# Performance work log

Measured on AMD Instinct MI355X. Metric: run time of the kernel, lower is better.

## Reference

```python
import jax, jax.numpy as jnp
import numpy as np

N_NODES = 100000


def gcn_conv(x, edge_index, edge_weight, W, b):
    """PyG GCNConv: out = D^-1/2 (A + I) D^-1/2 X W + b (self-loop weight 1)."""
    n = x.shape[0]
    src, dst = edge_index[0], edge_index[1]
    loop = jnp.arange(n)
    src_sl = jnp.concatenate([src, loop])
    dst_sl = jnp.concatenate([dst, loop])
    ew_sl = jnp.concatenate([edge_weight, jnp.ones((n,), x.dtype)])
    deg = jax.ops.segment_sum(ew_sl, dst_sl, num_segments=n)  # [N]
    dinv = jnp.where(deg > 0, jax.lax.rsqrt(deg), 0.0)
    norm = dinv[src_sl] * ew_sl * dinv[dst_sl]  # [E+N]
    h = x @ W  # [N, out_dim] dense transform before propagation
    msg = h[src_sl] * norm[:, None]  # gather + scale, [E+N, out_dim]
    out = jax.ops.segment_sum(msg, dst_sl, num_segments=n)  # scatter-add
    return out + b


def setup_inputs() -> dict:
    key = jax.random.key(0)
    ks = jax.random.split(key, 9)
    in_dim, hidden, latent = 128, 64, 32
    n, e = N_NODES, 1600000
    x = jax.random.normal(ks[0], (n, in_dim), dtype=jnp.float32)
    edge_index = jax.random.randint(ks[1], (2, e), 0, n, dtype=jnp.int64)
    edge_weight = jax.random.uniform(ks[2], (e,), dtype=jnp.float32)
    def glorot(k, fan_in, fan_out):
        s = jnp.sqrt(6.0 / (fan_in + fan_out))
        return jax.random.uniform(k, (fan_in, fan_out), jnp.float32, -s, s)
    return {
        "x": x,
        "edge_index": edge_index,
        "edge_weight": edge_weight,
        "W1": glorot(ks[3], in_dim, hidden),
        "b1": jnp.zeros((hidden,), jnp.float32),
        "W_mu": glorot(ks[4], hidden, latent),
        "b_mu": jnp.zeros((latent,), jnp.float32),
        "W_lv": glorot(ks[5], hidden, latent),
        "b_lv": jnp.zeros((latent,), jnp.float32),
    }


def reference(x, edge_index, edge_weight, W1, b1, W_mu, b_mu, W_lv, b_lv):
    h = jax.nn.relu(gcn_conv(x, edge_index, edge_weight, W1, b1))
    mu = gcn_conv(h, edge_index, edge_weight, W_mu, b_mu)
    logvar = gcn_conv(h, edge_index, edge_weight, W_lv, b_lv)
    return (mu, logvar)
```

## Files before the change

### kernel.cpp

```cpp
#include <hip/hip_runtime.h>

static __device__ __forceinline__ float4 ld4(const float* p) { return *(const float4*)p; }
static __device__ __forceinline__ float b2f(unsigned short u) {
    return __uint_as_float((unsigned)u << 16);
}
static __device__ __forceinline__ float b2f_lo(unsigned u) { return __uint_as_float(u << 16); }
static __device__ __forceinline__ float b2f_hi(unsigned u) { return __uint_as_float(u & 0xFFFF0000u); }
static __device__ __forceinline__ unsigned short f2b(float f) {
    unsigned x = __float_as_uint(f);
    return (unsigned short)((x + 0x7FFFu + ((x >> 16) & 1u)) >> 16);
}
static __device__ __forceinline__ unsigned pk2(float lo, float hi) {
    return (unsigned)f2b(lo) | ((unsigned)f2b(hi) << 16);
}

typedef __attribute__((ext_vector_type(8))) short bf16x8;
typedef __attribute__((ext_vector_type(4))) float f32x4;

#define NPB 256
#define CAPE 5120



__global__ __launch_bounds__(256) void k_prep(const float* __restrict__ W1,
                                              const float* __restrict__ Wmu,
                                              const float* __restrict__ Wlv,
                                              unsigned short* __restrict__ Wf1,
                                              unsigned short* __restrict__ Wf2) {
    int tid = threadIdx.x;
    if (blockIdx.x == 0) {
        for (int idx = tid; idx < 2048; idx += 256) {
            int frag = idx >> 6, lane = idx & 63;
            int s = frag & 1, ct = (frag >> 1) & 3, kb = frag >> 3;
            int rA = lane & 15, g8 = (lane >> 4) * 8;
            int c = ct * 16 + rA;
            unsigned short* dstp = Wf1 + frag * 512 + lane * 8;
            for (int j = 0; j < 8; j++) {
                float wv = W1[(size_t)(kb * 32 + g8 + j) * 64 + c];
                unsigned short hi = f2b(wv);
                dstp[j] = (s == 0) ? hi : f2b(wv - b2f(hi));
            }
        }
    } else {
        for (int idx = tid; idx < 1024; idx += 256) {
            int frag = idx >> 6, lane = idx & 63;
            int s = frag & 1, ct = (frag >> 1) & 3, kb = frag >> 3;
            int rA = lane & 15, g8 = (lane >> 4) * 8;
            int c = ct * 16 + rA;
            int k0 = kb * 32 + g8;
            unsigned short* dstp = Wf2 + frag * 512 + lane * 8;
            for (int j = 0; j < 8; j++) {
                float wv = (c < 32) ? Wmu[(size_t)(k0 + j) * 32 + c]
                                    : Wlv[(size_t)(k0 + j) * 32 + (c - 32)];
                unsigned short hi = f2b(wv);
                dstp[j] = (s == 0) ? hi : f2b(wv - b2f(hi));
            }
        }
    }
}

static __device__ __forceinline__ void split8(const float* xv, bf16x8& ah, bf16x8& al) {
    #pragma unroll
    for (int j = 0; j < 8; j++) {
        unsigned u = __float_as_uint(xv[j]);
        float res = xv[j] - __uint_as_float(u & 0xFFFF0000u);
        ah[j] = (short)(u >> 16);
        al[j] = (short)(__float_as_uint(res) >> 16);
    }
}

__global__ __launch_bounds__(256) void k_fused1(const float* __restrict__ A,
                                                const unsigned short* __restrict__ Wf1,
                                                unsigned short* __restrict__ gout,
                                                const int* __restrict__ src,
                                                const int* __restrict__ dst,
                                                const float* __restrict__ ew,
                                                int* __restrict__ bin_cnt,
                                                unsigned long long* __restrict__ ebuf,
                                                int n, int E, int gb, int NB) {
    __shared__ int hist[512];
    __shared__ int hbase[512];
    int tid = threadIdx.x;

    if ((int)blockIdx.x < gb) {
        int row0 = blockIdx.x * 64;
        int w = tid >> 6, lane = tid & 63;
        int rA = lane & 15, g8 = (lane >> 4) * 8;
        int row = row0 + w * 16 + rA;
        const float* xr = A + (size_t)min(row, n - 1) * 128;
        f32x4 acc[4] = {{0.f, 0.f, 0.f, 0.f}, {0.f, 0.f, 0.f, 0.f},
                        {0.f, 0.f, 0.f, 0.f}, {0.f, 0.f, 0.f, 0.f}};
        #pragma unroll
        for (int kb = 0; kb < 4; kb++) {
            float4 v0 = ld4(xr + kb * 32 + g8);
            float4 v1 = ld4(xr + kb * 32 + g8 + 4);
            float xv[8] = {v0.x, v0.y, v0.z, v0.w, v1.x, v1.y, v1.z, v1.w};
            bf16x8 ah, al;
            split8(xv, ah, al);
            const unsigned short* wb = Wf1 + (size_t)(kb * 8) * 512 + lane * 8;
            #pragma unroll
            for (int ct = 0; ct < 4; ct++) {
                bf16x8 bh = *(const bf16x8*)(wb + (ct * 2 + 0) * 512);
                bf16x8 bl = *(const bf16x8*)(wb + (ct * 2 + 1) * 512);
                acc[ct] = __builtin_amdgcn_mfma_f32_16x16x32_bf16(ah, bh, acc[ct], 0, 0, 0);
                acc[ct] = __builtin_amdgcn_mfma_f32_16x16x32_bf16(al, bh, acc[ct], 0, 0, 0);
                acc[ct] = __builtin_amdgcn_mfma_f32_16x16x32_bf16(ah, bl, acc[ct], 0, 0, 0);
            }
        }
        int rbase = row0 + w * 16 + (lane >> 4) * 4;
        #pragma unroll
        for (int reg = 0; reg < 4; reg++) {
            int grow = rbase + reg;
            if (grow < n) {
                #pragma unroll
                for (int ct = 0; ct < 4; ct++)
                    gout[(size_t)grow * 64 + ct * 16 + rA] = f2b(acc[ct][reg]);
            }
        }
    } else {
        for (int j = tid; j < NB; j += 256) hist[j] = 0;
        __syncthreads();
        int e0 = ((int)blockIdx.x - gb) * 4096;
        unsigned long long pk[16]; int bb[16]; int loc[16];
        #pragma unroll
        for (int j = 0; j < 16; j++) {
            int e = e0 + j * 256 + tid;
            if (e < E) {
                int s = src[e];
                int d = dst[e];
                float w = ew[e];
                bb[j] = d >> 8;
                pk[j] = ((unsigned long long)__float_as_uint(w) << 32) |
                        (unsigned)((d & (NPB - 1)) << 17) | (unsigned)s;
                loc[j] = atomicAdd(&hist[bb[j]], 1);
            } else bb[j] = -1;
        }
        __syncthreads();
        for (int j = tid; j < NB; j += 256) hbase[j] = atomicAdd(&bin_cnt[j], hist[j]);
        __syncthreads();
        #pragma unroll
        for (int j = 0; j < 16; j++) {
            if (bb[j] >= 0)
                ebuf[(size_t)bb[j] * CAPE + hbase[bb[j]] + loc[j]] = pk[j];
        }
    }
}

__global__ __launch_bounds__(512) void k_csr_build(const unsigned long long* __restrict__ ebuf,
                                                   const int* __restrict__ bin_cnt,
                                                   int2* __restrict__ rowcnt,
                                                   float* __restrict__ dinv,
                                                   unsigned long long* __restrict__ csr,
                                                   unsigned short* __restrict__ h0,
                                                   int n) {
    __shared__ unsigned long long eL[CAPE];
    __shared__ unsigned cntL[NPB];
    __shared__ unsigned ewsL[NPB];
    __shared__ unsigned fillL[NPB];
    __shared__ int scanL[512];
    __shared__ int rowL[NPB];
    __shared__ float dinvL[NPB];
    __shared__ int binbase_s;
    int b = blockIdx.x;
    int tid = threadIdx.x;
    if (tid < NPB) { cntL[tid] = 0; ewsL[tid] = 0; fillL[tid] = 0; }
    scanL[tid] = (tid < b) ? bin_cnt[tid] : 0;
    __syncthreads();
    int m = bin_cnt[b];
    const unsigned long long* eb = ebuf + (size_t)b * CAPE;
    for (int i = tid; i < m; i += 512) {
        unsigned long long pk = eb[i];
        eL[i] = pk;
        int ld = (int)((pk >> 17) & (NPB - 1));
        float w = __uint_as_float((unsigned)(pk >> 32));
        atomicAdd(&cntL[ld], 1u);
        atomicAdd(&ewsL[ld], (unsigned)(w * 16777216.0f));
    }
    __syncthreads();
    #pragma unroll
    for (int off = 256; off > 0; off >>= 1) {
        if (tid < off) scanL[tid] += scanL[tid + off];
        __syncthreads();
    }
    if (tid == 0) binbase_s = scanL[0];
    __syncthreads();
    int v = (tid < NPB) ? (int)cntL[tid] : 0;
    scanL[tid] = v;
    __syncthreads();
    #pragma unroll
    for (int off = 1; off < 512; off <<= 1) {
        int t = (tid >= off) ? scanL[tid - off] : 0;
        __syncthreads();
        scanL[tid] += t;
        __syncthreads();
    }
    if (tid < NPB) {
        int rp = binbase_s + scanL[tid] - v;
        rowL[tid] = rp;
        float dv = rsqrtf(1.0f + (float)ewsL[tid] * (1.0f / 16777216.0f));
        dinvL[tid] = dv;
        int node = b * NPB + tid;
        if (node < n) {
            rowcnt[node] = make_int2(rp, v);
            dinv[node] = dv;
        }
    }
    __syncthreads();
    for (int i = tid; i < m; i += 512) {
        unsigned long long pk = eL[i];
        int s = (int)(pk & 0x1FFFF);
        int ld = (int)((pk >> 17) & (NPB - 1));
        int pos = rowL[ld] + (int)atomicAdd(&fillL[ld], 1u);
        csr[pos] = (unsigned long long)(unsigned)s | (pk & 0xFFFFFFFF00000000ull);
    }
    for (int idx = tid; idx < NPB * 8; idx += 512) {
        int ln = idx >> 3;
        int node = b * NPB + ln;
        if (node < n) {
            float sc = dinvL[ln];
            unsigned short* hp = h0 + (size_t)node * 64 + (idx & 7) * 8;
            uint4 u = *(uint4*)hp;
            u.x = pk2(b2f_lo(u.x) * sc, b2f_hi(u.x) * sc);
            u.y = pk2(b2f_lo(u.y) * sc, b2f_hi(u.y) * sc);
            u.z = pk2(b2f_lo(u.z) * sc, b2f_hi(u.z) * sc);
            u.w = pk2(b2f_lo(u.w) * sc, b2f_hi(u.w) * sc);
            *(uint4*)hp = u;
        }
    }
}

__global__ __launch_bounds__(256) void k_gemm2(const unsigned short* __restrict__ h,
                                               const unsigned short* __restrict__ Wf2,
                                               const float* __restrict__ dinv,
                                               unsigned short* __restrict__ out, int n) {
    int tid = threadIdx.x;
    int row0 = blockIdx.x * 64;
    int w = tid >> 6, lane = tid & 63;
    int rA = lane & 15, g8 = (lane >> 4) * 8;
    int row = row0 + w * 16 + rA;
    const unsigned short* hr = h + (size_t)min(row, n - 1) * 64;
    f32x4 acc[4] = {{0.f, 0.f, 0.f, 0.f}, {0.f, 0.f, 0.f, 0.f},
                    {0.f, 0.f, 0.f, 0.f}, {0.f, 0.f, 0.f, 0.f}};
    #pragma unroll
    for (int kb = 0; kb < 2; kb++) {
        bf16x8 a = *(const bf16x8*)(hr + kb * 32 + g8);
        const unsigned short* wb = Wf2 + (size_t)(kb * 8) * 512 + lane * 8;
        #pragma unroll
        for (int ct = 0; ct < 4; ct++) {
            bf16x8 bh = *(const bf16x8*)(wb + (ct * 2 + 0) * 512);
            bf16x8 bl = *(const bf16x8*)(wb + (ct * 2 + 1) * 512);
            acc[ct] = __builtin_amdgcn_mfma_f32_16x16x32_bf16(a, bh, acc[ct], 0, 0, 0);
            acc[ct] = __builtin_amdgcn_mfma_f32_16x16x32_bf16(a, bl, acc[ct], 0, 0, 0);
        }
    }
    int rbase = row0 + w * 16 + (lane >> 4) * 4;
    #pragma unroll
    for (int reg = 0; reg < 4; reg++) {
        int grow = rbase + reg;
        if (grow < n) {
            float sc = dinv[grow];
            #pragma unroll
            for (int ct = 0; ct < 4; ct++)
                out[(size_t)grow * 64 + ct * 16 + rA] = f2b(acc[ct][reg] * sc);
        }
    }
}

static __device__ __forceinline__ void acc8(float* a, uint4 r, float wt) {
    a[0] = fmaf(b2f_lo(r.x), wt, a[0]); a[1] = fmaf(b2f_hi(r.x), wt, a[1]);
    a[2] = fmaf(b2f_lo(r.y), wt, a[2]); a[3] = fmaf(b2f_hi(r.y), wt, a[3]);
    a[4] = fmaf(b2f_lo(r.z), wt, a[4]); a[5] = fmaf(b2f_hi(r.z), wt, a[5]);
    a[6] = fmaf(b2f_lo(r.w), wt, a[6]); a[7] = fmaf(b2f_hi(r.w), wt, a[7]);
}

template<bool RELU, bool SPLIT_OUT>
__global__ __launch_bounds__(256) void k_prop(const unsigned short* __restrict__ g,
                                              const int2* __restrict__ csr,
                                              const int2* __restrict__ rowcnt,
                                              const float* __restrict__ dinv,
                                              const float* __restrict__ bias0,
                                              const float* __restrict__ bias1,
                                              void* __restrict__ outv, int n) {
    int node = blockIdx.x * 4 + (threadIdx.x >> 6);
    if (node >= n) return;
    int lane = threadIdx.x & 63;
    int q = lane >> 3;
    int t = lane & 7;
    uint4 sr = *(const uint4*)(g + (size_t)node * 64 + t * 8);
    int2 rc = rowcnt[node];
    const int2* ep = csr + rc.x;
    int m = rc.y;
    float a[8] = {};
    for (int e = 0; e < m; e += 32) {
        int e1 = e + q, e2 = e1 + 8, e3 = e1 + 16, e4 = e1 + 24;
        int i1 = min(e1, m - 1), i2 = min(e2, m - 1);
        int i3 = min(e3, m - 1), i4 = min(e4, m - 1);
        int2 p1 = ep[i1];
        int2 p2 = ep[i2];
        int2 p3 = ep[i3];
        int2 p4 = ep[i4];
        uint4 r1 = *(const uint4*)(g + (size_t)p1.x * 64 + t * 8);
        uint4 r2 = *(const uint4*)(g + (size_t)p2.x * 64 + t * 8);
        uint4 r3 = *(const uint4*)(g + (size_t)p3.x * 64 + t * 8);
        uint4 r4 = *(const uint4*)(g + (size_t)p4.x * 64 + t * 8);
        float w1 = (e1 < m) ? __int_as_float(p1.y) : 0.f;
        float w2 = (e2 < m) ? __int_as_float(p2.y) : 0.f;
        float w3 = (e3 < m) ? __int_as_float(p3.y) : 0.f;
        float w4 = (e4 < m) ? __int_as_float(p4.y) : 0.f;
        acc8(a, r1, w1);
        acc8(a, r2, w2);
        acc8(a, r3, w3);
        acc8(a, r4, w4);
    }
    #pragma unroll
    for (int i = 0; i < 8; i++) {
        a[i] += __shfl_xor(a[i], 8);
        a[i] += __shfl_xor(a[i], 16);
        a[i] += __shfl_xor(a[i], 32);
    }
    if (q != 0) return;
    a[0] += b2f_lo(sr.x); a[1] += b2f_hi(sr.x);
    a[2] += b2f_lo(sr.y); a[3] += b2f_hi(sr.y);
    a[4] += b2f_lo(sr.z); a[5] += b2f_hi(sr.z);
    a[6] += b2f_lo(sr.w); a[7] += b2f_hi(sr.w);
    float di = dinv[node];
    #pragma unroll
    for (int i = 0; i < 8; i++) a[i] *= di;
    if (!SPLIT_OUT) {
        float4 b0 = ld4(bias0 + t * 8);
        float4 b1 = ld4(bias0 + t * 8 + 4);
        a[0] += b0.x; a[1] += b0.y; a[2] += b0.z; a[3] += b0.w;
        a[4] += b1.x; a[5] += b1.y; a[6] += b1.z; a[7] += b1.w;
        if (RELU) {
            #pragma unroll
            for (int i = 0; i < 8; i++) a[i] = fmaxf(a[i], 0.f);
        }
        uint4 u = make_uint4(pk2(a[0], a[1]), pk2(a[2], a[3]),
                             pk2(a[4], a[5]), pk2(a[6], a[7]));
        *(uint4*)((unsigned short*)outv + (size_t)node * 64 + t * 8) = u;
    } else {
        float* out = (float*)outv;
        const float* bp = (t < 4) ? (bias0 + t * 8) : (bias1 + (t - 4) * 8);
        size_t base = (t < 4) ? ((size_t)node * 32 + t * 8)
                              : ((size_t)n * 32 + (size_t)node * 32 + (t - 4) * 8);
        float4 b0 = ld4(bp);
        float4 b1 = ld4(bp + 4);
        float4 v0 = make_float4(a[0] + b0.x, a[1] + b0.y, a[2] + b0.z, a[3] + b0.w);
        float4 v1 = make_float4(a[4] + b1.x, a[5] + b1.y, a[6] + b1.z, a[7] + b1.w);
        *(float4*)&out[base] = v0;
        *(float4*)&out[base + 4] = v1;
    }
}

extern "C" void kernel_launch(void* const* d_in, const int* in_sizes, int n_in,
                              void* d_out, int out_size, void* d_ws, size_t ws_size,
                              hipStream_t stream) {
    const float* x   = (const float*)d_in[0];
    const int*   ei  = (const int*)d_in[1];
    const float* ew  = (const float*)d_in[2];
    const float* W1  = (const float*)d_in[3];
    const float* b1  = (const float*)d_in[4];
    const float* Wmu = (const float*)d_in[5];
    const float* bmu = (const float*)d_in[6];
    const float* Wlv = (const float*)d_in[7];
    const float* blv = (const float*)d_in[8];
    float* outp = (float*)d_out;

    const int n = in_sizes[0] / 128;
    const int E = in_sizes[2];
    const int* src = ei;
    const int* dst = ei + E;
    const int NB = (n + NPB - 1) / NPB;

    size_t o = 0;
    auto alloc = [&](size_t bytes) { void* p = (char*)d_ws + o; o += (bytes + 511) & ~(size_t)511; return p; };
    int*   bin_cnt  = (int*)alloc((size_t)NB * 4);
    int2*  rowcnt   = (int2*)alloc((size_t)n * 8);
    float* dinv     = (float*)alloc((size_t)n * 4);
    unsigned long long* csr  = (unsigned long long*)alloc((size_t)E * 8);
    unsigned long long* ebuf = (unsigned long long*)alloc((size_t)NB * CAPE * 8);
    unsigned short* g0 = (unsigned short*)alloc((size_t)n * 64 * 2);
    unsigned short* h  = (unsigned short*)alloc((size_t)n * 64 * 2);
    unsigned short* Wf1 = (unsigned short*)alloc(32 * 512 * 2);
    unsigned short* Wf2 = (unsigned short*)alloc(16 * 512 * 2);
    unsigned short* g2 = g0;

    const int gb = (n + 63) / 64;
    const int bb = (E + 4095) / 4096;

    k_prep<<<2, 256, 0, stream>>>(W1, Wmu, Wlv, Wf1, Wf2);
    hipMemsetAsync(bin_cnt, 0, (size_t)NB * 4, stream);
    k_fused1<<<gb + bb, 256, 0, stream>>>(x, Wf1, g0, src, dst, ew,
                                          bin_cnt, ebuf, n, E, gb, NB);
    k_csr_build<<<NB, 512, 0, stream>>>(ebuf, bin_cnt, rowcnt, dinv, csr, g0, n);
    k_prop<true, false><<<(n + 3) / 4, 256, 0, stream>>>(g0, (const int2*)csr, rowcnt, dinv,
                                                         b1, nullptr, h, n);
    k_gemm2<<<gb, 256, 0, stream>>>(h, Wf2, dinv, g2, n);
    k_prop<false, true><<<(n + 3) / 4, 256, 0, stream>>>(g2, (const int2*)csr, rowcnt, dinv,
                                                         bmu, blv, outp, n);
}
```

Measured before the change: 278.3 us.

## Move source-side dinv scaling into first propagation and widen GEMM row tiles

The pass in csr_build that rescaled g0 rows by dinv is removed. The first propagation kernel now multiplies each edge weight by dinv of its source node through a gather, which saves a read-modify-write over the whole feature matrix but adds a random dinv load per edge. It also adds a fast path for nodes with at most 16 edges. In addition, both MFMA GEMMs process 128 rows per block instead of 64, and fused1 now schedules the binning blocks before the GEMM blocks.

```diff
diff --git a/kernel.cpp b/kernel.cpp
--- a/kernel.cpp
+++ b/kernel.cpp
@@ -77,34 +77,43 @@
                                                 const float* __restrict__ ew,
                                                 int* __restrict__ bin_cnt,
                                                 unsigned long long* __restrict__ ebuf,
-                                                int n, int E, int gb, int NB) {
+                                                int n, int E, int bb_cnt, int NB) {
     __shared__ int hist[512];
     __shared__ int hbase[512];
     int tid = threadIdx.x;
 
-    if ((int)blockIdx.x < gb) {
-        int row0 = blockIdx.x * 64;
+    if ((int)blockIdx.x >= bb_cnt) {
+        int row0 = ((int)blockIdx.x - bb_cnt) * 128;
         int w = tid >> 6, lane = tid & 63;
         int rA = lane & 15, g8 = (lane >> 4) * 8;
-        int row = row0 + w * 16 + rA;
-        const float* xr = A + (size_t)min(row, n - 1) * 128;
-        f32x4 acc[4] = {{0.f, 0.f, 0.f, 0.f}, {0.f, 0.f, 0.f, 0.f},
-                        {0.f, 0.f, 0.f, 0.f}, {0.f, 0.f, 0.f, 0.f}};
+        int rowa = row0 + w * 16 + rA;
+        int rowb = rowa + 64;
+        const float* xa = A + (size_t)min(rowa, n - 1) * 128;
+        const float* xb = A + (size_t)min(rowb, n - 1) * 128;
+        f32x4 acc0[4] = {{0.f,0.f,0.f,0.f},{0.f,0.f,0.f,0.f},{0.f,0.f,0.f,0.f},{0.f,0.f,0.f,0.f}};
+        f32x4 acc1[4] = {{0.f,0.f,0.f,0.f},{0.f,0.f,0.f,0.f},{0.f,0.f,0.f,0.f},{0.f,0.f,0.f,0.f}};
         #pragma unroll
         for (int kb = 0; kb < 4; kb++) {
-            float4 v0 = ld4(xr + kb * 32 + g8);
-            float4 v1 = ld4(xr + kb * 32 + g8 + 4);
-            float xv[8] = {v0.x, v0.y, v0.z, v0.w, v1.x, v1.y, v1.z, v1.w};
-            bf16x8 ah, al;
-            split8(xv, ah, al);
+            float4 va0 = ld4(xa + kb * 32 + g8);
+            float4 va1 = ld4(xa + kb * 32 + g8 + 4);
+            float4 vb0 = ld4(xb + kb * 32 + g8);
+            float4 vb1 = ld4(xb + kb * 32 + g8 + 4);
+            float xva[8] = {va0.x, va0.y, va0.z, va0.w, va1.x, va1.y, va1.z, va1.w};
+            float xvb[8] = {vb0.x, vb0.y, vb0.z, vb0.w, vb1.x, vb1.y, vb1.z, vb1.w};
+            bf16x8 ahA, alA, ahB, alB;
+            split8(xva, ahA, alA);
+            split8(xvb, ahB, alB);
             const unsigned short* wb = Wf1 + (size_t)(kb * 8) * 512 + lane * 8;
             #pragma unroll
             for (int ct = 0; ct < 4; ct++) {
                 bf16x8 bh = *(const bf16x8*)(wb + (ct * 2 + 0) * 512);
                 bf16x8 bl = *(const bf16x8*)(wb + (ct * 2 + 1) * 512);
-                acc[ct] = __builtin_amdgcn_mfma_f32_16x16x32_bf16(ah, bh, acc[ct], 0, 0, 0);
-                acc[ct] = __builtin_amdgcn_mfma_f32_16x16x32_bf16(al, bh, acc[ct], 0, 0, 0);
-                acc[ct] = __builtin_amdgcn_mfma_f32_16x16x32_bf16(ah, bl, acc[ct], 0, 0, 0);
+                acc0[ct] = __builtin_amdgcn_mfma_f32_16x16x32_bf16(ahA, bh, acc0[ct], 0, 0, 0);
+                acc0[ct] = __builtin_amdgcn_mfma_f32_16x16x32_bf16(alA, bh, acc0[ct], 0, 0, 0);
+                acc0[ct] = __builtin_amdgcn_mfma_f32_16x16x32_bf16(ahA, bl, acc0[ct], 0, 0, 0);
+                acc1[ct] = __builtin_amdgcn_mfma_f32_16x16x32_bf16(ahB, bh, acc1[ct], 0, 0, 0);
+                acc1[ct] = __builtin_amdgcn_mfma_f32_16x16x32_bf16(alB, bh, acc1[ct], 0, 0, 0);
+                acc1[ct] = __builtin_amdgcn_mfma_f32_16x16x32_bf16(ahB, bl, acc1[ct], 0, 0, 0);
             }
         }
         int rbase = row0 + w * 16 + (lane >> 4) * 4;
@@ -114,13 +123,19 @@
             if (grow < n) {
                 #pragma unroll
                 for (int ct = 0; ct < 4; ct++)
-                    gout[(size_t)grow * 64 + ct * 16 + rA] = f2b(acc[ct][reg]);
+                    gout[(size_t)grow * 64 + ct * 16 + rA] = f2b(acc0[ct][reg]);
+            }
+            int grow2 = grow + 64;
+            if (grow2 < n) {
+                #pragma unroll
+                for (int ct = 0; ct < 4; ct++)
+                    gout[(size_t)grow2 * 64 + ct * 16 + rA] = f2b(acc1[ct][reg]);
             }
         }
     } else {
         for (int j = tid; j < NB; j += 256) hist[j] = 0;
         __syncthreads();
-        int e0 = ((int)blockIdx.x - gb) * 4096;
+        int e0 = (int)blockIdx.x * 4096;
         unsigned long long pk[16]; int bb[16]; int loc[16];
         #pragma unroll
         for (int j = 0; j < 16; j++) {
@@ -151,7 +166,6 @@
                                                    int2* __restrict__ rowcnt,
                                                    float* __restrict__ dinv,
                                                    unsigned long long* __restrict__ csr,
-                                                   unsigned short* __restrict__ h0,
                                                    int n) {
     __shared__ unsigned long long eL[CAPE];
     __shared__ unsigned cntL[NPB];
@@ -159,7 +173,6 @@
     __shared__ unsigned fillL[NPB];
     __shared__ int scanL[512];
     __shared__ int rowL[NPB];
-    __shared__ float dinvL[NPB];
     __shared__ int binbase_s;
     int b = blockIdx.x;
     int tid = threadIdx.x;
@@ -197,12 +210,10 @@
     if (tid < NPB) {
         int rp = binbase_s + scanL[tid] - v;
         rowL[tid] = rp;
-        float dv = rsqrtf(1.0f + (float)ewsL[tid] * (1.0f / 16777216.0f));
-        dinvL[tid] = dv;
         int node = b * NPB + tid;
         if (node < n) {
             rowcnt[node] = make_int2(rp, v);
-            dinv[node] = dv;
+            dinv[node] = rsqrtf(1.0f + (float)ewsL[tid] * (1.0f / 16777216.0f));
         }
     }
     __syncthreads();
@@ -213,20 +224,6 @@
         int pos = rowL[ld] + (int)atomicAdd(&fillL[ld], 1u);
         csr[pos] = (unsigned long long)(unsigned)s | (pk & 0xFFFFFFFF00000000ull);
     }
-    for (int idx = tid; idx < NPB * 8; idx += 512) {
-        int ln = idx >> 3;
-        int node = b * NPB + ln;
-        if (node < n) {
-            float sc = dinvL[ln];
-            unsigned short* hp = h0 + (size_t)node * 64 + (idx & 7) * 8;
-            uint4 u = *(uint4*)hp;
-            u.x = pk2(b2f_lo(u.x) * sc, b2f_hi(u.x) * sc);
-            u.y = pk2(b2f_lo(u.y) * sc, b2f_hi(u.y) * sc);
-            u.z = pk2(b2f_lo(u.z) * sc, b2f_hi(u.z) * sc);
-            u.w = pk2(b2f_lo(u.w) * sc, b2f_hi(u.w) * sc);
-            *(uint4*)hp = u;
-        }
-    }
 }
 
 __global__ __launch_bounds__(256) void k_gemm2(const unsigned short* __restrict__ h,
@@ -234,23 +231,28 @@
                                                const float* __restrict__ dinv,
                                                unsigned short* __restrict__ out, int n) {
     int tid = threadIdx.x;
-    int row0 = blockIdx.x * 64;
+    int row0 = blockIdx.x * 128;
     int w = tid >> 6, lane = tid & 63;
     int rA = lane & 15, g8 = (lane >> 4) * 8;
-    int row = row0 + w * 16 + rA;
-    const unsigned short* hr = h + (size_t)min(row, n - 1) * 64;
-    f32x4 acc[4] = {{0.f, 0.f, 0.f, 0.f}, {0.f, 0.f, 0.f, 0.f},
-                    {0.f, 0.f, 0.f, 0.f}, {0.f, 0.f, 0.f, 0.f}};
+    int rowa = row0 + w * 16 + rA;
+    int rowb = rowa + 64;
+    const unsigned short* ha = h + (size_t)min(rowa, n - 1) * 64;
+    const unsigned short* hb = h + (size_t)min(rowb, n - 1) * 64;
+    f32x4 acc0[4] = {{0.f,0.f,0.f,0.f},{0.f,0.f,0.f,0.f},{0.f,0.f,0.f,0.f},{0.f,0.f,0.f,0.f}};
+    f32x4 acc1[4] = {{0.f,0.f,0.f,0.f},{0.f,0.f,0.f,0.f},{0.f,0.f,0.f,0.f},{0.f,0.f,0.f,0.f}};
     #pragma unroll
     for (int kb = 0; kb < 2; kb++) {
-        bf16x8 a = *(const bf16x8*)(hr + kb * 32 + g8);
+        bf16x8 aA = *(const bf16x8*)(ha + kb * 32 + g8);
+        bf16x8 aB = *(const bf16x8*)(hb + kb * 32 + g8);
         const unsigned short* wb = Wf2 + (size_t)(kb * 8) * 512 + lane * 8;
         #pragma unroll
         for (int ct = 0; ct < 4; ct++) {
             bf16x8 bh = *(const bf16x8*)(wb + (ct * 2 + 0) * 512);
             bf16x8 bl = *(const bf16x8*)(wb + (ct * 2 + 1) * 512);
-            acc[ct] = __builtin_amdgcn_mfma_f32_16x16x32_bf16(a, bh, acc[ct], 0, 0, 0);
-            acc[ct] = __builtin_amdgcn_mfma_f32_16x16x32_bf16(a, bl, acc[ct], 0, 0, 0);
+            acc0[ct] = __builtin_amdgcn_mfma_f32_16x16x32_bf16(aA, bh, acc0[ct], 0, 0, 0);
+            acc0[ct] = __builtin_amdgcn_mfma_f32_16x16x32_bf16(aA, bl, acc0[ct], 0, 0, 0);
+            acc1[ct] = __builtin_amdgcn_mfma_f32_16x16x32_bf16(aB, bh, acc1[ct], 0, 0, 0);
+            acc1[ct] = __builtin_amdgcn_mfma_f32_16x16x32_bf16(aB, bl, acc1[ct], 0, 0, 0);
         }
     }
     int rbase = row0 + w * 16 + (lane >> 4) * 4;
@@ -261,7 +263,14 @@
             float sc = dinv[grow];
             #pragma unroll
             for (int ct = 0; ct < 4; ct++)
-                out[(size_t)grow * 64 + ct * 16 + rA] = f2b(acc[ct][reg] * sc);
+                out[(size_t)grow * 64 + ct * 16 + rA] = f2b(acc0[ct][reg] * sc);
+        }
+        int grow2 = grow + 64;
+        if (grow2 < n) {
+            float sc = dinv[grow2];
+            #pragma unroll
+            for (int ct = 0; ct < 4; ct++)
+                out[(size_t)grow2 * 64 + ct * 16 + rA] = f2b(acc1[ct][reg] * sc);
         }
     }
 }
@@ -273,7 +282,7 @@
     a[6] = fmaf(b2f_lo(r.w), wt, a[6]); a[7] = fmaf(b2f_hi(r.w), wt, a[7]);
 }
 
-template<bool RELU, bool SPLIT_OUT>
+template<bool RELU, bool SPLIT_OUT, bool DSCALE>
 __global__ __launch_bounds__(256) void k_prop(const unsigned short* __restrict__ g,
                                               const int2* __restrict__ csr,
                                               const int2* __restrict__ rowcnt,
@@ -291,26 +300,44 @@
     const int2* ep = csr + rc.x;
     int m = rc.y;
     float a[8] = {};
-    for (int e = 0; e < m; e += 32) {
-        int e1 = e + q, e2 = e1 + 8, e3 = e1 + 16, e4 = e1 + 24;
+    if (m > 0 && m <= 16) {
+        int e1 = q, e2 = q + 8;
         int i1 = min(e1, m - 1), i2 = min(e2, m - 1);
-        int i3 = min(e3, m - 1), i4 = min(e4, m - 1);
         int2 p1 = ep[i1];
         int2 p2 = ep[i2];
-        int2 p3 = ep[i3];
-        int2 p4 = ep[i4];
         uint4 r1 = *(const uint4*)(g + (size_t)p1.x * 64 + t * 8);
         uint4 r2 = *(const uint4*)(g + (size_t)p2.x * 64 + t * 8);
-        uint4 r3 = *(const uint4*)(g + (size_t)p3.x * 64 + t * 8);
-        uint4 r4 = *(const uint4*)(g + (size_t)p4.x * 64 + t * 8);
         float w1 = (e1 < m) ? __int_as_float(p1.y) : 0.f;
         float w2 = (e2 < m) ? __int_as_float(p2.y) : 0.f;
-        float w3 = (e3 < m) ? __int_as_float(p3.y) : 0.f;
-        float w4 = (e4 < m) ? __int_as_float(p4.y) : 0.f;
+        if (DSCALE) { w1 *= dinv[p1.x]; w2 *= dinv[p2.x]; }
         acc8(a, r1, w1);
         acc8(a, r2, w2);
-        acc8(a, r3, w3);
-        acc8(a, r4, w4);
+    } else {
+        for (int e = 0; e < m; e += 32) {
+            int e1 = e + q, e2 = e1 + 8, e3 = e1 + 16, e4 = e1 + 24;
+            int i1 = min(e1, m - 1), i2 = min(e2, m - 1);
+            int i3 = min(e3, m - 1), i4 = min(e4, m - 1);
+            int2 p1 = ep[i1];
+            int2 p2 = ep[i2];
+            int2 p3 = ep[i3];
+            int2 p4 = ep[i4];
+            uint4 r1 = *(const uint4*)(g + (size_t)p1.x * 64 + t * 8);
+            uint4 r2 = *(const uint4*)(g + (size_t)p2.x * 64 + t * 8);
+            uint4 r3 = *(const uint4*)(g + (size_t)p3.x * 64 + t * 8);
+            uint4 r4 = *(const uint4*)(g + (size_t)p4.x * 64 + t * 8);
+            float w1 = (e1 < m) ? __int_as_float(p1.y) : 0.f;
+            float w2 = (e2 < m) ? __int_as_float(p2.y) : 0.f;
+            float w3 = (e3 < m) ? __int_as_float(p3.y) : 0.f;
+            float w4 = (e4 < m) ? __int_as_float(p4.y) : 0.f;
+            if (DSCALE) {
+                w1 *= dinv[p1.x]; w2 *= dinv[p2.x];
+                w3 *= dinv[p3.x]; w4 *= dinv[p4.x];
+            }
+            acc8(a, r1, w1);
+            acc8(a, r2, w2);
+            acc8(a, r3, w3);
+            acc8(a, r4, w4);
+        }
     }
     #pragma unroll
     for (int i = 0; i < 8; i++) {
@@ -319,11 +346,12 @@
         a[i] += __shfl_xor(a[i], 32);
     }
     if (q != 0) return;
-    a[0] += b2f_lo(sr.x); a[1] += b2f_hi(sr.x);
-    a[2] += b2f_lo(sr.y); a[3] += b2f_hi(sr.y);
-    a[4] += b2f_lo(sr.z); a[5] += b2f_hi(sr.z);
-    a[6] += b2f_lo(sr.w); a[7] += b2f_hi(sr.w);
     float di = dinv[node];
+    float ss = DSCALE ? di : 1.f;
+    a[0] += ss * b2f_lo(sr.x); a[1] += ss * b2f_hi(sr.x);
+    a[2] += ss * b2f_lo(sr.y); a[3] += ss * b2f_hi(sr.y);
+    a[4] += ss * b2f_lo(sr.z); a[5] += ss * b2f_hi(sr.z);
+    a[6] += ss * b2f_lo(sr.w); a[7] += ss * b2f_hi(sr.w);
     #pragma unroll
     for (int i = 0; i < 8; i++) a[i] *= di;
     if (!SPLIT_OUT) {
@@ -385,17 +413,17 @@
     unsigned short* Wf2 = (unsigned short*)alloc(16 * 512 * 2);
     unsigned short* g2 = g0;
 
-    const int gb = (n + 63) / 64;
+    const int gb = (n + 127) / 128;
     const int bb = (E + 4095) / 4096;
 
     k_prep<<<2, 256, 0, stream>>>(W1, Wmu, Wlv, Wf1, Wf2);
     hipMemsetAsync(bin_cnt, 0, (size_t)NB * 4, stream);
-    k_fused1<<<gb + bb, 256, 0, stream>>>(x, Wf1, g0, src, dst, ew,
-                                          bin_cnt, ebuf, n, E, gb, NB);
-    k_csr_build<<<NB, 512, 0, stream>>>(ebuf, bin_cnt, rowcnt, dinv, csr, g0, n);
-    k_prop<true, false><<<(n + 3) / 4, 256, 0, stream>>>(g0, (const int2*)csr, rowcnt, dinv,
-                                                         b1, nullptr, h, n);
-    k_gemm2<<<gb, 256, 0, stream>>>(h, Wf2, dinv, g2, n);
-    k_prop<false, true><<<(n + 3) / 4, 256, 0, stream>>>(g2, (const int2*)csr, rowcnt, dinv,
-                                                         bmu, blv, outp, n);
-}
+    k_fused1<<<bb + gb, 256, 0, stream>>>(x, Wf1, g0, src, dst, ew,
+                                          bin_cnt, ebuf, n, E, bb, NB);
+    k_csr_build<<<NB, 512, 0, stream>>>(ebuf, bin_cnt, rowcnt, dinv, csr, n);
+    k_prop<true, false, true><<<(n + 3) / 4, 256, 0, stream>>>(g0, (const int2*)csr, rowcnt, dinv,
+                                                               b1, nullptr, h, n);
+    k_gemm2<<<(n + 127) / 128, 256, 0, stream>>>(h, Wf2, dinv, g2, n);
+    k_prop<false, true, false><<<(n + 3) / 4, 256, 0, stream>>>(g2, (const int2*)csr, rowcnt, dinv,
+                                                                bmu, blv, outp, n);
+}
```

New measurement: 273.0 us. About the same (-1.9%).

## Fuse second GEMM into first propagation and drop in-place dinv prescale

Applied to the files above, without the earlier changes.

Fuses the hidden-to-latent GEMM into the first propagation kernel: each node's 64-wide hidden row is multiplied by an FP32 W2 held in LDS using wave shuffles, which removes the separate k_gemm2 launch and the round trip of h through memory. The source-side dinv scaling now happens per edge inside the gather instead of as a rescale pass over g0 in csr_build. The CSR base offset comes from an atomic counter rather than a per-block reduction, and the memset is folded into the prep kernel. A fast path handles rows with at most 16 edges. Costs: an extra dinv gather per edge, 64 shuffle-FMAs per lane per node in place of MFMA, and CSR row order now depends on atomic ordering.

```diff
diff --git a/kernel.cpp b/kernel.cpp
--- a/kernel.cpp
+++ b/kernel.cpp
@@ -26,7 +26,9 @@
                                               const float* __restrict__ Wmu,
                                               const float* __restrict__ Wlv,
                                               unsigned short* __restrict__ Wf1,
-                                              unsigned short* __restrict__ Wf2) {
+                                              float* __restrict__ W2cat,
+                                              int* __restrict__ bin_cnt,
+                                              int* __restrict__ ctr, int NB) {
     int tid = threadIdx.x;
     if (blockIdx.x == 0) {
         for (int idx = tid; idx < 2048; idx += 256) {
@@ -41,21 +43,14 @@
                 dstp[j] = (s == 0) ? hi : f2b(wv - b2f(hi));
             }
         }
+    } else if (blockIdx.x == 1) {
+        for (int idx = tid; idx < 4096; idx += 256) {
+            int k = idx >> 6, c = idx & 63;
+            W2cat[idx] = (c < 32) ? Wmu[(size_t)k * 32 + c] : Wlv[(size_t)k * 32 + (c - 32)];
+        }
     } else {
-        for (int idx = tid; idx < 1024; idx += 256) {
-            int frag = idx >> 6, lane = idx & 63;
-            int s = frag & 1, ct = (frag >> 1) & 3, kb = frag >> 3;
-            int rA = lane & 15, g8 = (lane >> 4) * 8;
-            int c = ct * 16 + rA;
-            int k0 = kb * 32 + g8;
-            unsigned short* dstp = Wf2 + frag * 512 + lane * 8;
-            for (int j = 0; j < 8; j++) {
-                float wv = (c < 32) ? Wmu[(size_t)(k0 + j) * 32 + c]
-                                    : Wlv[(size_t)(k0 + j) * 32 + (c - 32)];
-                unsigned short hi = f2b(wv);
-                dstp[j] = (s == 0) ? hi : f2b(wv - b2f(hi));
-            }
-        }
+        for (int j = tid; j < NB; j += 256) bin_cnt[j] = 0;
+        if (tid == 0) *ctr = 0;
     }
 }
 
@@ -81,15 +76,15 @@
     __shared__ int hist[512];
     __shared__ int hbase[512];
     int tid = threadIdx.x;
-
-    if ((int)blockIdx.x < gb) {
-        int row0 = blockIdx.x * 64;
+    int bid = blockIdx.x;
+
+    if (bid < gb) {
+        int row0 = bid * 64;
         int w = tid >> 6, lane = tid & 63;
         int rA = lane & 15, g8 = (lane >> 4) * 8;
         int row = row0 + w * 16 + rA;
         const float* xr = A + (size_t)min(row, n - 1) * 128;
-        f32x4 acc[4] = {{0.f, 0.f, 0.f, 0.f}, {0.f, 0.f, 0.f, 0.f},
-                        {0.f, 0.f, 0.f, 0.f}, {0.f, 0.f, 0.f, 0.f}};
+        f32x4 acc[4] = {{0.f,0.f,0.f,0.f},{0.f,0.f,0.f,0.f},{0.f,0.f,0.f,0.f},{0.f,0.f,0.f,0.f}};
         #pragma unroll
         for (int kb = 0; kb < 4; kb++) {
             float4 v0 = ld4(xr + kb * 32 + g8);
@@ -120,7 +115,7 @@
     } else {
         for (int j = tid; j < NB; j += 256) hist[j] = 0;
         __syncthreads();
-        int e0 = ((int)blockIdx.x - gb) * 4096;
+        int e0 = (bid - gb) * 4096;
         unsigned long long pk[16]; int bb[16]; int loc[16];
         #pragma unroll
         for (int j = 0; j < 16; j++) {
@@ -148,10 +143,10 @@
 
 __global__ __launch_bounds__(512) void k_csr_build(const unsigned long long* __restrict__ ebuf,
                                                    const int* __restrict__ bin_cnt,
+                                                   int* __restrict__ ctr,
                                                    int2* __restrict__ rowcnt,
                                                    float* __restrict__ dinv,
                                                    unsigned long long* __restrict__ csr,
-                                                   unsigned short* __restrict__ h0,
                                                    int n) {
     __shared__ unsigned long long eL[CAPE];
     __shared__ unsigned cntL[NPB];
@@ -159,14 +154,13 @@
     __shared__ unsigned fillL[NPB];
     __shared__ int scanL[512];
     __shared__ int rowL[NPB];
-    __shared__ float dinvL[NPB];
     __shared__ int binbase_s;
     int b = blockIdx.x;
     int tid = threadIdx.x;
     if (tid < NPB) { cntL[tid] = 0; ewsL[tid] = 0; fillL[tid] = 0; }
-    scanL[tid] = (tid < b) ? bin_cnt[tid] : 0;
     __syncthreads();
     int m = bin_cnt[b];
+    if (tid == 0) binbase_s = atomicAdd(ctr, m);
     const unsigned long long* eb = ebuf + (size_t)b * CAPE;
     for (int i = tid; i < m; i += 512) {
         unsigned long long pk = eb[i];
@@ -177,13 +171,6 @@
         atomicAdd(&ewsL[ld], (unsigned)(w * 16777216.0f));
     }
     __syncthreads();
-    #pragma unroll
-    for (int off = 256; off > 0; off >>= 1) {
-        if (tid < off) scanL[tid] += scanL[tid + off];
-        __syncthreads();
-    }
-    if (tid == 0) binbase_s = scanL[0];
-    __syncthreads();
     int v = (tid < NPB) ? (int)cntL[tid] : 0;
     scanL[tid] = v;
     __syncthreads();
@@ -197,12 +184,10 @@
     if (tid < NPB) {
         int rp = binbase_s + scanL[tid] - v;
         rowL[tid] = rp;
-        float dv = rsqrtf(1.0f + (float)ewsL[tid] * (1.0f / 16777216.0f));
-        dinvL[tid] = dv;
         int node = b * NPB + tid;
         if (node < n) {
             rowcnt[node] = make_int2(rp, v);
-            dinv[node] = dv;
+            dinv[node] = rsqrtf(1.0f + (float)ewsL[tid] * (1.0f / 16777216.0f));
         }
     }
     __syncthreads();
@@ -213,57 +198,6 @@
         int pos = rowL[ld] + (int)atomicAdd(&fillL[ld], 1u);
         csr[pos] = (unsigned long long)(unsigned)s | (pk & 0xFFFFFFFF00000000ull);
     }
-    for (int idx = tid; idx < NPB * 8; idx += 512) {
-        int ln = idx >> 3;
-        int node = b * NPB + ln;
-        if (node < n) {
-            float sc = dinvL[ln];
-            unsigned short* hp = h0 + (size_t)node * 64 + (idx & 7) * 8;
-            uint4 u = *(uint4*)hp;
-            u.x = pk2(b2f_lo(u.x) * sc, b2f_hi(u.x) * sc);
-            u.y = pk2(b2f_lo(u.y) * sc, b2f_hi(u.y) * sc);
-            u.z = pk2(b2f_lo(u.z) * sc, b2f_hi(u.z) * sc);
-            u.w = pk2(b2f_lo(u.w) * sc, b2f_hi(u.w) * sc);
-            *(uint4*)hp = u;
-        }
-    }
-}
-
-__global__ __launch_bounds__(256) void k_gemm2(const unsigned short* __restrict__ h,
-                                               const unsigned short* __restrict__ Wf2,
-                                               const float* __restrict__ dinv,
-                                               unsigned short* __restrict__ out, int n) {
-    int tid = threadIdx.x;
-    int row0 = blockIdx.x * 64;
-    int w = tid >> 6, lane = tid & 63;
-    int rA = lane & 15, g8 = (lane >> 4) * 8;
-    int row = row0 + w * 16 + rA;
-    const unsigned short* hr = h + (size_t)min(row, n - 1) * 64;
-    f32x4 acc[4] = {{0.f, 0.f, 0.f, 0.f}, {0.f, 0.f, 0.f, 0.f},
-                    {0.f, 0.f, 0.f, 0.f}, {0.f, 0.f, 0.f, 0.f}};
-    #pragma unroll
-    for (int kb = 0; kb < 2; kb++) {
-        bf16x8 a = *(const bf16x8*)(hr + kb * 32 + g8);
-        const unsigned short* wb = Wf2 + (size_t)(kb * 8) * 512 + lane * 8;
-        #pragma unroll
-        for (int ct = 0; ct < 4; ct++) {
-            bf16x8 bh = *(const bf16x8*)(wb + (ct * 2 + 0) * 512);
-            bf16x8 bl = *(const bf16x8*)(wb + (ct * 2 + 1) * 512);
-            acc[ct] = __builtin_amdgcn_mfma_f32_16x16x32_bf16(a, bh, acc[ct], 0, 0, 0);
-            acc[ct] = __builtin_amdgcn_mfma_f32_16x16x32_bf16(a, bl, acc[ct], 0, 0, 0);
-        }
-    }
-    int rbase = row0 + w * 16 + (lane >> 4) * 4;
-    #pragma unroll
-    for (int reg = 0; reg < 4; reg++) {
-        int grow = rbase + reg;
-        if (grow < n) {
-            float sc = dinv[grow];
-            #pragma unroll
-            for (int ct = 0; ct < 4; ct++)
-                out[(size_t)grow * 64 + ct * 16 + rA] = f2b(acc[ct][reg] * sc);
-        }
-    }
 }
 
 static __device__ __forceinline__ void acc8(float* a, uint4 r, float wt) {
@@ -273,14 +207,113 @@
     a[6] = fmaf(b2f_lo(r.w), wt, a[6]); a[7] = fmaf(b2f_hi(r.w), wt, a[7]);
 }
 
-template<bool RELU, bool SPLIT_OUT>
-__global__ __launch_bounds__(256) void k_prop(const unsigned short* __restrict__ g,
-                                              const int2* __restrict__ csr,
-                                              const int2* __restrict__ rowcnt,
-                                              const float* __restrict__ dinv,
-                                              const float* __restrict__ bias0,
-                                              const float* __restrict__ bias1,
-                                              void* __restrict__ outv, int n) {
+template<bool DSCALE>
+static __device__ __forceinline__ void gather_row(const unsigned short* g, const int2* ep,
+                                                  int m, int q, int t,
+                                                  const float* dinv, float* a) {
+    if (m > 0 && m <= 16) {
+        int e1 = q, e2 = q + 8;
+        int i1 = min(e1, m - 1), i2 = min(e2, m - 1);
+        int2 p1 = ep[i1];
+        int2 p2 = ep[i2];
+        uint4 r1 = *(const uint4*)(g + (size_t)p1.x * 64 + t * 8);
+        uint4 r2 = *(const uint4*)(g + (size_t)p2.x * 64 + t * 8);
+        float w1 = (e1 < m) ? __int_as_float(p1.y) : 0.f;
+        float w2 = (e2 < m) ? __int_as_float(p2.y) : 0.f;
+        if (DSCALE) { w1 *= dinv[p1.x]; w2 *= dinv[p2.x]; }
+        acc8(a, r1, w1);
+        acc8(a, r2, w2);
+    } else {
+        for (int e = 0; e < m; e += 32) {
+            int e1 = e + q, e2 = e1 + 8, e3 = e1 + 16, e4 = e1 + 24;
+            int i1 = min(e1, m - 1), i2 = min(e2, m - 1);
+            int i3 = min(e3, m - 1), i4 = min(e4, m - 1);
+            int2 p1 = ep[i1];
+            int2 p2 = ep[i2];
+            int2 p3 = ep[i3];
+            int2 p4 = ep[i4];
+            uint4 r1 = *(const uint4*)(g + (size_t)p1.x * 64 + t * 8);
+            uint4 r2 = *(const uint4*)(g + (size_t)p2.x * 64 + t * 8);
+            uint4 r3 = *(const uint4*)(g + (size_t)p3.x * 64 + t * 8);
+            uint4 r4 = *(const uint4*)(g + (size_t)p4.x * 64 + t * 8);
+            float w1 = (e1 < m) ? __int_as_float(p1.y) : 0.f;
+            float w2 = (e2 < m) ? __int_as_float(p2.y) : 0.f;
+            float w3 = (e3 < m) ? __int_as_float(p3.y) : 0.f;
+            float w4 = (e4 < m) ? __int_as_float(p4.y) : 0.f;
+            if (DSCALE) {
+                w1 *= dinv[p1.x]; w2 *= dinv[p2.x];
+                w3 *= dinv[p3.x]; w4 *= dinv[p4.x];
+            }
+            acc8(a, r1, w1);
+            acc8(a, r2, w2);
+            acc8(a, r3, w3);
+            acc8(a, r4, w4);
+        }
+    }
+}
+
+__global__ __launch_bounds__(512) void k_prop1g(const unsigned short* __restrict__ g,
+                                                const int2* __restrict__ csr,
+                                                const int2* __restrict__ rowcnt,
+                                                const float* __restrict__ dinv,
+                                                const float* __restrict__ bias0,
+                                                const float* __restrict__ W2cat,
+                                                unsigned short* __restrict__ g2, int n) {
+    __shared__ float W2s[4096];
+    int tid = threadIdx.x;
+    for (int j = tid; j < 1024; j += 512)
+        *(float4*)&W2s[j * 4] = ld4(W2cat + j * 4);
+    __syncthreads();
+    int node = blockIdx.x * 8 + (tid >> 6);
+    if (node >= n) return;
+    int lane = tid & 63;
+    int q = lane >> 3;
+    int t = lane & 7;
+    uint4 sr = *(const uint4*)(g + (size_t)node * 64 + t * 8);
+    int2 rc = rowcnt[node];
+    const int2* ep = csr + rc.x;
+    float a[8] = {};
+    gather_row<true>(g, ep, rc.y, q, t, dinv, a);
+    #pragma unroll
+    for (int i = 0; i < 8; i++) {
+        a[i] += __shfl_xor(a[i], 8);
+        a[i] += __shfl_xor(a[i], 16);
+        a[i] += __shfl_xor(a[i], 32);
+    }
+    float di = dinv[node];
+    a[0] += di * b2f_lo(sr.x); a[1] += di * b2f_hi(sr.x);
+    a[2] += di * b2f_lo(sr.y); a[3] += di * b2f_hi(sr.y);
+    a[4] += di * b2f_lo(sr.z); a[5] += di * b2f_hi(sr.z);
+    a[6] += di * b2f_lo(sr.w); a[7] += di * b2f_hi(sr.w);
+    float4 b0 = ld4(bias0 + t * 8);
+    float4 b1v = ld4(bias0 + t * 8 + 4);
+    a[0] = fmaxf(fmaf(a[0], di, b0.x), 0.f);
+    a[1] = fmaxf(fmaf(a[1], di, b0.y), 0.f);
+    a[2] = fmaxf(fmaf(a[2], di, b0.z), 0.f);
+    a[3] = fmaxf(fmaf(a[3], di, b0.w), 0.f);
+    a[4] = fmaxf(fmaf(a[4], di, b1v.x), 0.f);
+    a[5] = fmaxf(fmaf(a[5], di, b1v.y), 0.f);
+    a[6] = fmaxf(fmaf(a[6], di, b1v.z), 0.f);
+    a[7] = fmaxf(fmaf(a[7], di, b1v.w), 0.f);
+    float u = 0.f;
+    #pragma unroll
+    for (int j = 0; j < 8; j++) {
+        #pragma unroll
+        for (int t2 = 0; t2 < 8; t2++) {
+            float hv = __shfl(a[j], t2);
+            u = fmaf(hv, W2s[(t2 * 8 + j) * 64 + lane], u);
+        }
+    }
+    g2[(size_t)node * 64 + lane] = f2b(u * di);
+}
+
+__global__ __launch_bounds__(256) void k_prop2(const unsigned short* __restrict__ g,
+                                               const int2* __restrict__ csr,
+                                               const int2* __restrict__ rowcnt,
+                                               const float* __restrict__ dinv,
+                                               const float* __restrict__ bias0,
+                                               const float* __restrict__ bias1,
+                                               float* __restrict__ out, int n) {
     int node = blockIdx.x * 4 + (threadIdx.x >> 6);
     if (node >= n) return;
     int lane = threadIdx.x & 63;
@@ -289,29 +322,8 @@
     uint4 sr = *(const uint4*)(g + (size_t)node * 64 + t * 8);
     int2 rc = rowcnt[node];
     const int2* ep = csr + rc.x;
-    int m = rc.y;
     float a[8] = {};
-    for (int e = 0; e < m; e += 32) {
-        int e1 = e + q, e2 = e1 + 8, e3 = e1 + 16, e4 = e1 + 24;
-        int i1 = min(e1, m - 1), i2 = min(e2, m - 1);
-        int i3 = min(e3, m - 1), i4 = min(e4, m - 1);
-        int2 p1 = ep[i1];
-        int2 p2 = ep[i2];
-        int2 p3 = ep[i3];
-        int2 p4 = ep[i4];
-        uint4 r1 = *(const uint4*)(g + (size_t)p1.x * 64 + t * 8);
-        uint4 r2 = *(const uint4*)(g + (size_t)p2.x * 64 + t * 8);
-        uint4 r3 = *(const uint4*)(g + (size_t)p3.x * 64 + t * 8);
-        uint4 r4 = *(const uint4*)(g + (size_t)p4.x * 64 + t * 8);
-        float w1 = (e1 < m) ? __int_as_float(p1.y) : 0.f;
-        float w2 = (e2 < m) ? __int_as_float(p2.y) : 0.f;
-        float w3 = (e3 < m) ? __int_as_float(p3.y) : 0.f;
-        float w4 = (e4 < m) ? __int_as_float(p4.y) : 0.f;
-        acc8(a, r1, w1);
-        acc8(a, r2, w2);
-        acc8(a, r3, w3);
-        acc8(a, r4, w4);
-    }
+    gather_row<false>(g, ep, rc.y, q, t, nullptr, a);
     #pragma unroll
     for (int i = 0; i < 8; i++) {
         a[i] += __shfl_xor(a[i], 8);
@@ -326,30 +338,15 @@
     float di = dinv[node];
     #pragma unroll
     for (int i = 0; i < 8; i++) a[i] *= di;
-    if (!SPLIT_OUT) {
-        float4 b0 = ld4(bias0 + t * 8);
-        float4 b1 = ld4(bias0 + t * 8 + 4);
-        a[0] += b0.x; a[1] += b0.y; a[2] += b0.z; a[3] += b0.w;
-        a[4] += b1.x; a[5] += b1.y; a[6] += b1.z; a[7] += b1.w;
-        if (RELU) {
-            #pragma unroll
-            for (int i = 0; i < 8; i++) a[i] = fmaxf(a[i], 0.f);
-        }
-        uint4 u = make_uint4(pk2(a[0], a[1]), pk2(a[2], a[3]),
-                             pk2(a[4], a[5]), pk2(a[6], a[7]));
-        *(uint4*)((unsigned short*)outv + (size_t)node * 64 + t * 8) = u;
-    } else {
-        float* out = (float*)outv;
-        const float* bp = (t < 4) ? (bias0 + t * 8) : (bias1 + (t - 4) * 8);
-        size_t base = (t < 4) ? ((size_t)node * 32 + t * 8)
-                              : ((size_t)n * 32 + (size_t)node * 32 + (t - 4) * 8);
-        float4 b0 = ld4(bp);
-        float4 b1 = ld4(bp + 4);
-        float4 v0 = make_float4(a[0] + b0.x, a[1] + b0.y, a[2] + b0.z, a[3] + b0.w);
-        float4 v1 = make_float4(a[4] + b1.x, a[5] + b1.y, a[6] + b1.z, a[7] + b1.w);
-        *(float4*)&out[base] = v0;
-        *(float4*)&out[base + 4] = v1;
-    }
+    const float* bp = (t < 4) ? (bias0 + t * 8) : (bias1 + (t - 4) * 8);
+    size_t base = (t < 4) ? ((size_t)node * 32 + t * 8)
+                          : ((size_t)n * 32 + (size_t)node * 32 + (t - 4) * 8);
+    float4 b0 = ld4(bp);
+    float4 b1 = ld4(bp + 4);
+    float4 v0 = make_float4(a[0] + b0.x, a[1] + b0.y, a[2] + b0.z, a[3] + b0.w);
+    float4 v1 = make_float4(a[4] + b1.x, a[5] + b1.y, a[6] + b1.z, a[7] + b1.w);
+    *(float4*)&out[base] = v0;
+    *(float4*)&out[base + 4] = v1;
 }
 
 extern "C" void kernel_launch(void* const* d_in, const int* in_sizes, int n_in,
@@ -375,27 +372,25 @@
     size_t o = 0;
     auto alloc = [&](size_t bytes) { void* p = (char*)d_ws + o; o += (bytes + 511) & ~(size_t)511; return p; };
     int*   bin_cnt  = (int*)alloc((size_t)NB * 4);
+    int*   ctr      = (int*)alloc(512);
     int2*  rowcnt   = (int2*)alloc((size_t)n * 8);
     float* dinv     = (float*)alloc((size_t)n * 4);
     unsigned long long* csr  = (unsigned long long*)alloc((size_t)E * 8);
     unsigned long long* ebuf = (unsigned long long*)alloc((size_t)NB * CAPE * 8);
     unsigned short* g0 = (unsigned short*)alloc((size_t)n * 64 * 2);
-    unsigned short* h  = (unsigned short*)alloc((size_t)n * 64 * 2);
+    unsigned short* g2 = (unsigned short*)alloc((size_t)n * 64 * 2);
     unsigned short* Wf1 = (unsigned short*)alloc(32 * 512 * 2);
-    unsigned short* Wf2 = (unsigned short*)alloc(16 * 512 * 2);
-    unsigned short* g2 = g0;
+    float* W2cat = (float*)alloc(4096 * 4);
 
     const int gb = (n + 63) / 64;
     const int bb = (E + 4095) / 4096;
 
-    k_prep<<<2, 256, 0, stream>>>(W1, Wmu, Wlv, Wf1, Wf2);
-    hipMemsetAsync(bin_cnt, 0, (size_t)NB * 4, stream);
+    k_prep<<<3, 256, 0, stream>>>(W1, Wmu, Wlv, Wf1, W2cat, bin_cnt, ctr, NB);
     k_fused1<<<gb + bb, 256, 0, stream>>>(x, Wf1, g0, src, dst, ew,
                                           bin_cnt, ebuf, n, E, gb, NB);
-    k_csr_build<<<NB, 512, 0, stream>>>(ebuf, bin_cnt, rowcnt, dinv, csr, g0, n);
-    k_prop<true, false><<<(n + 3) / 4, 256, 0, stream>>>(g0, (const int2*)csr, rowcnt, dinv,
-                                                         b1, nullptr, h, n);
-    k_gemm2<<<gb, 256, 0, stream>>>(h, Wf2, dinv, g2, n);
-    k_prop<false, true><<<(n + 3) / 4, 256, 0, stream>>>(g2, (const int2*)csr, rowcnt, dinv,
-                                                         bmu, blv, outp, n);
-}
+    k_csr_build<<<NB, 512, 0, stream>>>(ebuf, bin_cnt, ctr, rowcnt, dinv, csr, n);
+    k_prop1g<<<(n + 7) / 8, 512, 0, stream>>>(g0, (const int2*)csr, rowcnt, dinv,
+                                              b1, W2cat, g2, n);
+    k_prop2<<<(n + 3) / 4, 256, 0, stream>>>(g2, (const int2*)csr, rowcnt, dinv,
+                                             bmu, blv, outp, n);
+}
```

Result: slower. 336.9 us (+21.1%).
